# Kernel optimization log

Measured on AMD Instinct MI355X. Metric: run time of the kernel, lower is better.

The kernel has to match this reference:

```python
import jax, jax.numpy as jnp
import numpy as np

D_MODEL = 512
D_STATE = 64
D_INNER = 2 * D_MODEL   # standard Mamba expand=2
D_CONV = 4
DT_RANK = D_MODEL // 16  # 32
LN_EPS = 1e-5


def setup_inputs() -> dict:
    key = jax.random.key(0)
    ks = jax.random.split(key, 12)
    B, L = 2, 1024
    s = 0.02
    return {
        "frames": jax.random.normal(ks[0], (B, L, D_MODEL), jnp.float32),
        "gamma": jnp.ones((D_MODEL,), jnp.float32),
        "beta": jnp.zeros((D_MODEL,), jnp.float32),
        "W_in": jax.random.normal(ks[1], (D_MODEL, 2 * D_INNER), jnp.float32) * s,
        "conv_w": jax.random.normal(ks[2], (D_INNER, D_CONV), jnp.float32) * s,
        "conv_b": jnp.zeros((D_INNER,), jnp.float32),
        "W_x": jax.random.normal(ks[3], (D_INNER, DT_RANK + 2 * D_STATE), jnp.float32) * s,
        "W_dt": jax.random.normal(ks[4], (DT_RANK, D_INNER), jnp.float32) * s,
        "b_dt": jax.random.uniform(ks[5], (D_INNER,), jnp.float32, -4.0, -2.0),
        "A_log": jnp.log(jnp.broadcast_to(jnp.arange(1, D_STATE + 1, dtype=jnp.float32), (D_INNER, D_STATE))),
        "D": jnp.ones((D_INNER,), jnp.float32),
        "W_out": jax.random.normal(ks[6], (D_INNER, D_MODEL), jnp.float32) * s,
    }


def reference(frames, gamma, beta, W_in, conv_w, conv_b, W_x, W_dt, b_dt, A_log, D, W_out):
    B, L, _ = frames.shape
    d_inner = W_in.shape[1] // 2
    d_state = A_log.shape[1]
    dt_rank = W_dt.shape[0]
    d_conv = conv_w.shape[1]

    # LayerNorm
    mu = frames.mean(-1, keepdims=True)
    var = ((frames - mu) ** 2).mean(-1, keepdims=True)
    xn = (frames - mu) * jax.lax.rsqrt(var + LN_EPS) * gamma + beta

    # in_proj -> x, z
    x, z = jnp.split(xn @ W_in, 2, axis=-1)  # each (B, L, d_inner)

    # causal depthwise conv1d along time
    xc = jnp.pad(x.transpose(0, 2, 1), ((0, 0), (0, 0), (d_conv - 1, 0)))  # (B, d_inner, L+pad)
    xconv = jax.lax.conv_general_dilated(
        xc, conv_w[:, None, :], (1,), "VALID", feature_group_count=d_inner)  # (B, d_inner, L)
    x = jax.nn.silu(xconv.transpose(0, 2, 1) + conv_b)  # (B, L, d_inner)

    # input-dependent dt, B, C
    xdb = x @ W_x
    dt, Bm, Cm = jnp.split(xdb, [dt_rank, dt_rank + d_state], axis=-1)
    delta = jax.nn.softplus(dt @ W_dt + b_dt)  # (B, L, d_inner)
    A = -jnp.exp(A_log)                        # (d_inner, d_state)

    # selective scan over time
    def step(h, inp):
        d_t, B_t, C_t, x_t = inp  # (B,d_inner) (B,d_state) (B,d_state) (B,d_inner)
        dA = jnp.exp(d_t[..., None] * A)                       # (B,d_inner,d_state)
        h = h * dA + (d_t * x_t)[..., None] * B_t[:, None, :]  # (B,d_inner,d_state)
        y = jnp.einsum("bds,bs->bd", h, C_t)
        return h, y

    h0 = jnp.zeros((B, d_inner, d_state), frames.dtype)
    xs = (delta.transpose(1, 0, 2), Bm.transpose(1, 0, 2),
          Cm.transpose(1, 0, 2), x.transpose(1, 0, 2))
    _, ys = jax.lax.scan(step, h0, xs)  # (L, B, d_inner)

    y = ys.transpose(1, 0, 2) + x * D
    y = y * jax.nn.silu(z)
    return y @ W_out + frames  # residual connection
```

## Files before the change

### kernel.cpp

```cpp
#include <hip/hip_runtime.h>
#include <hip/hip_bf16.h>
#include <math.h>

constexpr int Bn     = 2;
constexpr int Lseq   = 1024;
constexpr int DM     = 512;
constexpr int DI     = 1024;
constexpr int DS     = 64;
constexpr int RNK    = 32;
constexpr int NROWS  = Bn * Lseq;
constexpr int XDBW   = RNK + 2 * DS;
constexpr int CH     = 64;
constexpr int NC     = Lseq / CH;

typedef __attribute__((ext_vector_type(4))) float floatx4;
typedef __attribute__((ext_vector_type(8))) short shortx8;

__device__ __forceinline__ float silu_f(float v) {
    return v / (1.f + __expf(-v));
}

__device__ __forceinline__ float rdl(float v, int l) {
    return __int_as_float(__builtin_amdgcn_readlane(__float_as_int(v), l));
}

__global__ void ln_kernel(const float* __restrict__ x, const float* __restrict__ g,
                          const float* __restrict__ be, __hip_bfloat16* __restrict__ xn) {
    int row = blockIdx.x;
    int tid = threadIdx.x;
    const float* xr = x + (size_t)row * DM;
    float v0 = xr[tid], v1 = xr[tid + 256];
    float s = v0 + v1, sq = v0 * v0 + v1 * v1;
    #pragma unroll
    for (int o = 1; o < 64; o <<= 1) {
        s  += __shfl_xor(s, o);
        sq += __shfl_xor(sq, o);
    }
    __shared__ float red[8];
    int w = tid >> 6;
    if ((tid & 63) == 0) { red[w] = s; red[4 + w] = sq; }
    __syncthreads();
    float ts = red[0] + red[1] + red[2] + red[3];
    float tq = red[4] + red[5] + red[6] + red[7];
    float mu  = ts * (1.f / DM);
    float var = tq * (1.f / DM) - mu * mu;
    float inv = rsqrtf(var + 1e-5f);
    __hip_bfloat16* o0 = xn + (size_t)row * DM;
    o0[tid]       = __float2bfloat16((v0 - mu) * inv * g[tid]       + be[tid]);
    o0[tid + 256] = __float2bfloat16((v1 - mu) * inv * g[tid + 256] + be[tid + 256]);
}

__global__ void transpose_cast3(const float* __restrict__ Wi, const float* __restrict__ Wo,
                                const float* __restrict__ Wx,
                                __hip_bfloat16* __restrict__ Ti, __hip_bfloat16* __restrict__ To,
                                __hip_bfloat16* __restrict__ Tx) {
    __shared__ float tile[64][65];
    int bid = blockIdx.x;
    const float* in; __hip_bfloat16* out; int R, Cc, bx, by;
    if (bid < 256)      { in = Wi; out = Ti; R = DM; Cc = 2 * DI; bx = bid & 31;        by = bid >> 5; }
    else if (bid < 384) { int b2 = bid - 256; in = Wo; out = To; R = DI; Cc = DM;   bx = b2 & 7;  by = b2 >> 3; }
    else                { int b2 = bid - 384; in = Wx; out = Tx; R = DI; Cc = XDBW; bx = b2 % 3;  by = b2 / 3; }
    int r0 = by * 64, c0 = bx * 64;
    int tid = threadIdx.x;
    #pragma unroll
    for (int i = tid; i < 4096; i += 256) {
        int r = i >> 6, c = i & 63;
        tile[r][c] = (r0 + r < R && c0 + c < Cc) ? in[(size_t)(r0 + r) * Cc + c0 + c] : 0.f;
    }
    __syncthreads();
    #pragma unroll
    for (int i = tid; i < 4096; i += 256) {
        int c = i >> 6, r = i & 63;
        if (r0 + r < R && c0 + c < Cc)
            out[(size_t)(c0 + c) * R + r0 + r] = __float2bfloat16(tile[r][c]);
    }
}

template<bool RES>
__global__ __launch_bounds__(256) void gemm_bf16(const __hip_bfloat16* __restrict__ A,
                                                 const __hip_bfloat16* __restrict__ Bt,
                                                 const float* __restrict__ Res,
                                                 float* __restrict__ C,
                                                 int M, int N, int K) {
    __shared__ __hip_bfloat16 As[128 * 32];
    __shared__ __hip_bfloat16 Bs[128 * 32];
    const int tid  = threadIdx.x;
    const int wave = tid >> 6, lane = tid & 63;
    const int m0 = blockIdx.y * 128, n0 = blockIdx.x * 128;
    const int wm = (wave >> 1) * 64, wn = (wave & 1) * 64;

    floatx4 acc[4][4] = {};

    const int arow16 = lane & 15;
    const int kgrp   = lane >> 4;

    for (int k0 = 0; k0 < K; k0 += 32) {
        #pragma unroll
        for (int r = 0; r < 2; ++r) {
            int i   = wave * 64 + r * 256 + lane;
            int row = i >> 2, seg = i & 3;
            int brow = n0 + row; if (brow >= N) brow = N - 1;
            const __hip_bfloat16* gA = A  + (size_t)(m0 + row) * K + k0 + seg * 8;
            const __hip_bfloat16* gB = Bt + (size_t)brow * K + k0 + seg * 8;
            __hip_bfloat16* lA = As + (size_t)(wave * 64 + r * 256) * 8;
            __hip_bfloat16* lB = Bs + (size_t)(wave * 64 + r * 256) * 8;
            __builtin_amdgcn_global_load_lds(
                (const __attribute__((address_space(1))) void*)gA,
                (__attribute__((address_space(3))) void*)lA, 16, 0, 0);
            __builtin_amdgcn_global_load_lds(
                (const __attribute__((address_space(1))) void*)gB,
                (__attribute__((address_space(3))) void*)lB, 16, 0, 0);
        }
        __syncthreads();

        const shortx8* Asv = (const shortx8*)As;
        const shortx8* Bsv = (const shortx8*)Bs;
        shortx8 a[4], b[4];
        #pragma unroll
        for (int i = 0; i < 4; ++i)
            a[i] = Asv[(wm + i * 16 + arow16) * 4 + kgrp];
        #pragma unroll
        for (int j = 0; j < 4; ++j)
            b[j] = Bsv[(wn + j * 16 + arow16) * 4 + kgrp];
        #pragma unroll
        for (int i = 0; i < 4; ++i)
            #pragma unroll
            for (int j = 0; j < 4; ++j)
                acc[i][j] = __builtin_amdgcn_mfma_f32_16x16x32_bf16(a[i], b[j], acc[i][j], 0, 0, 0);
        __syncthreads();
    }

    const int drow = (lane >> 4) * 4;
    const int dcol = lane & 15;
    #pragma unroll
    for (int i = 0; i < 4; ++i)
        #pragma unroll
        for (int j = 0; j < 4; ++j) {
            int rowb = m0 + wm + i * 16 + drow;
            int col  = n0 + wn + j * 16 + dcol;
            if (col < N) {
                #pragma unroll
                for (int r = 0; r < 4; ++r) {
                    size_t idx = (size_t)(rowb + r) * N + col;
                    float v = acc[i][j][r];
                    if (RES) v += Res[idx];
                    C[idx] = v;
                }
            }
        }
}

template<bool RES>
__global__ __launch_bounds__(256) void gemm_bf16_64(const __hip_bfloat16* __restrict__ A,
                                                    const __hip_bfloat16* __restrict__ Bt,
                                                    const float* __restrict__ Res,
                                                    float* __restrict__ C,
                                                    int M, int N, int K) {
    __shared__ __hip_bfloat16 As[64 * 32];
    __shared__ __hip_bfloat16 Bs[64 * 32];
    const int tid  = threadIdx.x;
    const int wave = tid >> 6, lane = tid & 63;
    const int m0 = blockIdx.y * 64, n0 = blockIdx.x * 64;
    const int wm = (wave >> 1) * 32, wn = (wave & 1) * 32;

    floatx4 acc[2][2] = {};

    const int arow16 = lane & 15;
    const int kgrp   = lane >> 4;

    for (int k0 = 0; k0 < K; k0 += 32) {
        {
            int i   = wave * 64 + lane;
            int row = i >> 2, seg = i & 3;
            int brow = n0 + row; if (brow >= N) brow = N - 1;
            const __hip_bfloat16* gA = A  + (size_t)(m0 + row) * K + k0 + seg * 8;
            const __hip_bfloat16* gB = Bt + (size_t)brow * K + k0 + seg * 8;
            __hip_bfloat16* lA = As + (size_t)(wave * 64) * 8;
            __hip_bfloat16* lB = Bs + (size_t)(wave * 64) * 8;
            __builtin_amdgcn_global_load_lds(
                (const __attribute__((address_space(1))) void*)gA,
                (__attribute__((address_space(3))) void*)lA, 16, 0, 0);
            __builtin_amdgcn_global_load_lds(
                (const __attribute__((address_space(1))) void*)gB,
                (__attribute__((address_space(3))) void*)lB, 16, 0, 0);
        }
        __syncthreads();

        const shortx8* Asv = (const shortx8*)As;
        const shortx8* Bsv = (const shortx8*)Bs;
        shortx8 a[2], b[2];
        #pragma unroll
        for (int i = 0; i < 2; ++i)
            a[i] = Asv[(wm + i * 16 + arow16) * 4 + kgrp];
        #pragma unroll
        for (int j = 0; j < 2; ++j)
            b[j] = Bsv[(wn + j * 16 + arow16) * 4 + kgrp];
        #pragma unroll
        for (int i = 0; i < 2; ++i)
            #pragma unroll
            for (int j = 0; j < 2; ++j)
                acc[i][j] = __builtin_amdgcn_mfma_f32_16x16x32_bf16(a[i], b[j], acc[i][j], 0, 0, 0);
        __syncthreads();
    }

    const int drow = (lane >> 4) * 4;
    const int dcol = lane & 15;
    #pragma unroll
    for (int i = 0; i < 2; ++i)
        #pragma unroll
        for (int j = 0; j < 2; ++j) {
            int rowb = m0 + wm + i * 16 + drow;
            int col  = n0 + wn + j * 16 + dcol;
            if (col < N) {
                #pragma unroll
                for (int r = 0; r < 4; ++r) {
                    size_t idx = (size_t)(rowb + r) * N + col;
                    float v = acc[i][j][r];
                    if (RES) v += Res[idx];
                    C[idx] = v;
                }
            }
        }
}

__global__ void conv_silu(const float* __restrict__ xz, const float* __restrict__ cw,
                          const float* __restrict__ cb, float* __restrict__ xcv,
                          __hip_bfloat16* __restrict__ xcv_bf) {
    int idx = blockIdx.x * 256 + threadIdx.x;
    int d = idx & (DI - 1);
    int bt = idx / DI;
    int t = bt & (Lseq - 1);
    int b = bt / Lseq;
    float acc = cb[d];
    #pragma unroll
    for (int k = 0; k < 4; ++k) {
        int tt = t - 3 + k;
        float xv = (tt >= 0) ? xz[((size_t)(b * Lseq + tt)) * (2 * DI) + d] : 0.f;
        acc += xv * cw[d * 4 + k];
    }
    float v = silu_f(acc);
    xcv[idx] = v;
    xcv_bf[idx] = __float2bfloat16(v);
}

__global__ void delta_kernel(const float* __restrict__ xdb, const float* __restrict__ Wdt,
                             const float* __restrict__ bdt, float* __restrict__ delta) {
    int row = blockIdx.y;
    int d = blockIdx.x * 256 + threadIdx.x;
    __shared__ float dtv[RNK];
    if (threadIdx.x < RNK) dtv[threadIdx.x] = xdb[(size_t)row * XDBW + threadIdx.x];
    __syncthreads();
    float acc = bdt[d];
    #pragma unroll
    for (int r = 0; r < RNK; ++r) acc += dtv[r] * Wdt[(size_t)r * DI + d];
    float sp = (acc > 20.f) ? acc : log1pf(__expf(acc));
    delta[(size_t)row * DI + d] = sp;
}

__global__ __launch_bounds__(512) void scan_chunk1(
        const float* __restrict__ delta, const float* __restrict__ xcv,
        const float* __restrict__ xdb, const float* __restrict__ A_log,
        float* __restrict__ hend, float* __restrict__ dsum) {
    __shared__ float Bsh[64][68];
    __shared__ float dsh[8][64];
    __shared__ float xsh[8][64];

    int blk = blockIdx.x;
    int dg  = blk & (DI / 8 - 1);
    int bc  = blk >> 7;
    int c = bc & (NC - 1), b = bc >> 4;
    int tid = threadIdx.x, w = tid >> 6, lane = tid & 63;
    int d = dg * 8 + w;
    int r0 = b * Lseq + c * CH;

    #pragma unroll
    for (int k = 0; k < 2; ++k) {
        int idx = tid + k * 512;
        int row = idx >> 4, j4 = idx & 15;
        float4 v = *(const float4*)&xdb[(size_t)(r0 + row) * XDBW + RNK + j4 * 4];
        *(float4*)&Bsh[row][j4 * 4] = v;
    }
    {
        int t = tid >> 3, ww = tid & 7;
        dsh[ww][t] = delta[(size_t)(r0 + t) * DI + dg * 8 + ww];
        xsh[ww][t] = xcv[(size_t)(r0 + t) * DI + dg * 8 + ww];
    }
    __syncthreads();

    float a = -__expf(A_log[d * DS + lane]);
    float vd  = dsh[w][lane];
    float vpx = vd * xsh[w][lane];
    float h = 0.f;
    #pragma unroll 16
    for (int t = 0; t < CH; ++t) {
        float dt_ = rdl(vd, t);
        float px  = rdl(vpx, t);
        h = h * __expf(dt_ * a) + px * Bsh[t][lane];
    }
    float S = vd;
    #pragma unroll
    for (int o = 1; o < 64; o <<= 1) S += __shfl_xor(S, o);
    size_t base = ((size_t)bc * DI + d) * 64;
    hend[base + lane] = h;
    if (lane == 0) dsum[(size_t)bc * DI + d] = S;
}

__global__ __launch_bounds__(256) void scan_stitch(
        const float* __restrict__ hend, const float* __restrict__ dsum,
        const float* __restrict__ A_log, float* __restrict__ hstart) {
    int idx = blockIdx.x * 4 + (threadIdx.x >> 6);
    int lane = threadIdx.x & 63;
    int b = idx >> 10, d = idx & (DI - 1);
    float a = -__expf(A_log[d * DS + lane]);
    float h = 0.f;
    #pragma unroll
    for (int c = 0; c < NC; ++c) {
        size_t base = ((size_t)(b * NC + c) * DI + d) * 64;
        hstart[base + lane] = h;
        float he = hend[base + lane];
        float S  = dsum[(size_t)(b * NC + c) * DI + d];
        h = he + __expf(a * S) * h;
    }
}

__global__ __launch_bounds__(512) void scan_chunk2(
        const float* __restrict__ delta, const float* __restrict__ xcv,
        const float* __restrict__ xdb, const float* __restrict__ xz,
        const float* __restrict__ A_log, const float* __restrict__ Dp,
        const float* __restrict__ hstart, __hip_bfloat16* __restrict__ y_row) {
    __shared__ unsigned int BCsh[64][65];
    __shared__ float dsh[8][64];
    __shared__ float xsh[8][64];
    __shared__ float zsh[8][64];
    __shared__ float P[8][8 * 65];

    int blk = blockIdx.x;
    int dg  = blk & (DI / 8 - 1);
    int bc  = blk >> 7;
    int c = bc & (NC - 1), b = bc >> 4;
    int tid = threadIdx.x, w = tid >> 6, lane = tid & 63;
    int d = dg * 8 + w;
    int r0 = b * Lseq + c * CH;

    #pragma unroll
    for (int k = 0; k < 2; ++k) {
        int i = tid + k * 512;
        int t = i >> 4, sg = i & 15;
        const float* rowp = &xdb[(size_t)(r0 + t) * XDBW + RNK];
        float4 bv = *(const float4*)&rowp[sg * 4];
        float4 cv = *(const float4*)&rowp[DS + sg * 4];
        uint4 pk;
        #pragma unroll
        for (int j = 0; j < 4; ++j) {
            unsigned int bb = __float_as_uint((&bv.x)[j]);
            unsigned int cc2 = __float_as_uint((&cv.x)[j]);
            (&pk.x)[j] = (cc2 & 0xFFFF0000u) | (bb >> 16);
        }
        *(uint4*)&BCsh[t][sg * 4] = pk;
    }
    {
        int t = tid >> 3, ww = tid & 7;
        dsh[ww][t] = delta[(size_t)(r0 + t) * DI + dg * 8 + ww];
        xsh[ww][t] = xcv[(size_t)(r0 + t) * DI + dg * 8 + ww];
        zsh[ww][t] = xz[(size_t)(r0 + t) * (2 * DI) + DI + dg * 8 + ww];
    }
    __syncthreads();

    float a  = -__expf(A_log[d * DS + lane]);
    float Dv = Dp[d];
    float vd  = dsh[w][lane];
    float vpx = vd * xsh[w][lane];
    float h = hstart[((size_t)bc * DI + d) * 64 + lane];
    float* Pw = P[w];
    float yreg = 0.f;
    const int tr = lane & 7, q = lane >> 3;

    #pragma unroll
    for (int t8 = 0; t8 < 8; ++t8) {
        #pragma unroll
        for (int tt = 0; tt < 8; ++tt) {
            int t = t8 * 8 + tt;
            unsigned int bcp = BCsh[t][lane];
            float Bt = __uint_as_float(bcp << 16);
            float Ct = __uint_as_float(bcp & 0xFFFF0000u);
            float dt_ = rdl(vd, t);
            float px  = rdl(vpx, t);
            h = h * __expf(dt_ * a) + px * Bt;
            Pw[tt * 65 + lane] = h * Ct;
        }
        float sacc = 0.f;
        #pragma unroll
        for (int j = 0; j < 8; ++j) sacc += Pw[tr * 65 + q * 8 + j];
        sacc += __shfl_xor(sacc, 8);
        sacc += __shfl_xor(sacc, 16);
        sacc += __shfl_xor(sacc, 32);
        if (q == t8) yreg = sacc;
    }

    float yv = (yreg + xsh[w][lane] * Dv) * silu_f(zsh[w][lane]);

    __syncthreads();
    float* T = (float*)P;
    T[lane * 9 + w] = yv;
    __syncthreads();
    {
        int t = tid >> 3, dd = tid & 7;
        float v = T[t * 9 + dd];
        y_row[(size_t)(r0 + t) * DI + dg * 8 + dd] = __float2bfloat16(v);
    }
}

extern "C" void kernel_launch(void* const* d_in, const int* in_sizes, int n_in,
                              void* d_out, int out_size, void* d_ws, size_t ws_size,
                              hipStream_t stream) {
    const float* frames = (const float*)d_in[0];
    const float* gamma  = (const float*)d_in[1];
    const float* beta   = (const float*)d_in[2];
    const float* W_in   = (const float*)d_in[3];
    const float* conv_w = (const float*)d_in[4];
    const float* conv_b = (const float*)d_in[5];
    const float* W_x    = (const float*)d_in[6];
    const float* W_dt   = (const float*)d_in[7];
    const float* b_dt   = (const float*)d_in[8];
    const float* A_log  = (const float*)d_in[9];
    const float* Dp     = (const float*)d_in[10];
    const float* W_out  = (const float*)d_in[11];
    float* out = (float*)d_out;

    char* ws = (char*)d_ws;
    __hip_bfloat16* xn_bf  = (__hip_bfloat16*)ws; ws += (size_t)NROWS * DM * 2;
    __hip_bfloat16* Wt_in  = (__hip_bfloat16*)ws; ws += (size_t)(2 * DI) * DM * 2;
    __hip_bfloat16* Wt_out = (__hip_bfloat16*)ws; ws += (size_t)DM * DI * 2;
    __hip_bfloat16* Wt_x   = (__hip_bfloat16*)ws; ws += (size_t)XDBW * DI * 2;
    __hip_bfloat16* y_row  = (__hip_bfloat16*)ws; ws += (size_t)NROWS * DI * 2;
    __hip_bfloat16* xcv_bf = (__hip_bfloat16*)ws; ws += (size_t)NROWS * DI * 2;
    float* xz     = (float*)ws;  ws += (size_t)NROWS * 2 * DI * 4;
    float* xcv    = (float*)ws;  ws += (size_t)NROWS * DI * 4;
    float* xdb    = (float*)ws;  ws += (size_t)NROWS * XDBW * 4;
    float* delta  = (float*)ws;  ws += (size_t)NROWS * DI * 4;
    float* hend   = (float*)ws;  ws += (size_t)Bn * NC * DI * 64 * 4;
    float* hstart = (float*)ws;  ws += (size_t)Bn * NC * DI * 64 * 4;
    float* dsum   = (float*)ws;  ws += (size_t)Bn * NC * DI * 4;

    transpose_cast3<<<432, 256, 0, stream>>>(W_in, W_out, W_x, Wt_in, Wt_out, Wt_x);

    ln_kernel<<<NROWS, 256, 0, stream>>>(frames, gamma, beta, xn_bf);

    gemm_bf16<false><<<dim3(2 * DI / 128, NROWS / 128), 256, 0, stream>>>(
        xn_bf, Wt_in, nullptr, xz, NROWS, 2 * DI, DM);

    conv_silu<<<(NROWS * DI) / 256, 256, 0, stream>>>(xz, conv_w, conv_b, xcv, xcv_bf);

    gemm_bf16_64<false><<<dim3((XDBW + 63) / 64, NROWS / 64), 256, 0, stream>>>(
        xcv_bf, Wt_x, nullptr, xdb, NROWS, XDBW, DI);

    delta_kernel<<<dim3(DI / 256, NROWS), 256, 0, stream>>>(xdb, W_dt, b_dt, delta);

    scan_chunk1<<<Bn * NC * (DI / 8), 512, 0, stream>>>(delta, xcv, xdb, A_log, hend, dsum);
    scan_stitch<<<Bn * DI / 4, 256, 0, stream>>>(hend, dsum, A_log, hstart);
    scan_chunk2<<<Bn * NC * (DI / 8), 512, 0, stream>>>(delta, xcv, xdb, xz, A_log, Dp, hstart, y_row);

    gemm_bf16_64<true><<<dim3(DM / 64, NROWS / 64), 256, 0, stream>>>(
        y_row, Wt_out, frames, out, NROWS, DM, DI);
}
```

Measured before the change: 246.9 us.

## Use 512-thread GEMMs with intra-block split-K for small-N projections

The in_proj GEMM now runs with 8 waves per 128x128 tile, each wave owning a 64x32 sub-tile, so every block has more waves to hide latency. The x_proj and out_proj GEMMs switch to a split-K kernel: two groups of 4 waves each handle half of K with separate LDS buffers, and the partial sums are reduced through shared memory before the store. This targets the low occupancy and long serial K loop of the small-grid GEMMs, at the cost of extra LDS use, a reduction step, and more per-block synchronisation.

```diff
diff --git a/kernel.cpp b/kernel.cpp
--- a/kernel.cpp
+++ b/kernel.cpp
@@ -77,100 +77,26 @@
 }
 
 template<bool RES>
-__global__ __launch_bounds__(256) void gemm_bf16(const __hip_bfloat16* __restrict__ A,
-                                                 const __hip_bfloat16* __restrict__ Bt,
-                                                 const float* __restrict__ Res,
-                                                 float* __restrict__ C,
-                                                 int M, int N, int K) {
+__global__ __launch_bounds__(512) void gemm_bf16_512(const __hip_bfloat16* __restrict__ A,
+                                                     const __hip_bfloat16* __restrict__ Bt,
+                                                     const float* __restrict__ Res,
+                                                     float* __restrict__ C,
+                                                     int M, int N, int K) {
     __shared__ __hip_bfloat16 As[128 * 32];
     __shared__ __hip_bfloat16 Bs[128 * 32];
     const int tid  = threadIdx.x;
     const int wave = tid >> 6, lane = tid & 63;
     const int m0 = blockIdx.y * 128, n0 = blockIdx.x * 128;
-    const int wm = (wave >> 1) * 64, wn = (wave & 1) * 64;
-
-    floatx4 acc[4][4] = {};
+    const int wm = (wave >> 2) * 64, wn = (wave & 3) * 32;
+
+    floatx4 acc[4][2] = {};
 
     const int arow16 = lane & 15;
     const int kgrp   = lane >> 4;
 
     for (int k0 = 0; k0 < K; k0 += 32) {
-        #pragma unroll
-        for (int r = 0; r < 2; ++r) {
-            int i   = wave * 64 + r * 256 + lane;
-            int row = i >> 2, seg = i & 3;
-            int brow = n0 + row; if (brow >= N) brow = N - 1;
-            const __hip_bfloat16* gA = A  + (size_t)(m0 + row) * K + k0 + seg * 8;
-            const __hip_bfloat16* gB = Bt + (size_t)brow * K + k0 + seg * 8;
-            __hip_bfloat16* lA = As + (size_t)(wave * 64 + r * 256) * 8;
-            __hip_bfloat16* lB = Bs + (size_t)(wave * 64 + r * 256) * 8;
-            __builtin_amdgcn_global_load_lds(
-                (const __attribute__((address_space(1))) void*)gA,
-                (__attribute__((address_space(3))) void*)lA, 16, 0, 0);
-            __builtin_amdgcn_global_load_lds(
-                (const __attribute__((address_space(1))) void*)gB,
-                (__attribute__((address_space(3))) void*)lB, 16, 0, 0);
-        }
-        __syncthreads();
-
-        const shortx8* Asv = (const shortx8*)As;
-        const shortx8* Bsv = (const shortx8*)Bs;
-        shortx8 a[4], b[4];
-        #pragma unroll
-        for (int i = 0; i < 4; ++i)
-            a[i] = Asv[(wm + i * 16 + arow16) * 4 + kgrp];
-        #pragma unroll
-        for (int j = 0; j < 4; ++j)
-            b[j] = Bsv[(wn + j * 16 + arow16) * 4 + kgrp];
-        #pragma unroll
-        for (int i = 0; i < 4; ++i)
-            #pragma unroll
-            for (int j = 0; j < 4; ++j)
-                acc[i][j] = __builtin_amdgcn_mfma_f32_16x16x32_bf16(a[i], b[j], acc[i][j], 0, 0, 0);
-        __syncthreads();
-    }
-
-    const int drow = (lane >> 4) * 4;
-    const int dcol = lane & 15;
-    #pragma unroll
-    for (int i = 0; i < 4; ++i)
-        #pragma unroll
-        for (int j = 0; j < 4; ++j) {
-            int rowb = m0 + wm + i * 16 + drow;
-            int col  = n0 + wn + j * 16 + dcol;
-            if (col < N) {
-                #pragma unroll
-                for (int r = 0; r < 4; ++r) {
-                    size_t idx = (size_t)(rowb + r) * N + col;
-                    float v = acc[i][j][r];
-                    if (RES) v += Res[idx];
-                    C[idx] = v;
-                }
-            }
-        }
-}
-
-template<bool RES>
-__global__ __launch_bounds__(256) void gemm_bf16_64(const __hip_bfloat16* __restrict__ A,
-                                                    const __hip_bfloat16* __restrict__ Bt,
-                                                    const float* __restrict__ Res,
-                                                    float* __restrict__ C,
-                                                    int M, int N, int K) {
-    __shared__ __hip_bfloat16 As[64 * 32];
-    __shared__ __hip_bfloat16 Bs[64 * 32];
-    const int tid  = threadIdx.x;
-    const int wave = tid >> 6, lane = tid & 63;
-    const int m0 = blockIdx.y * 64, n0 = blockIdx.x * 64;
-    const int wm = (wave >> 1) * 32, wn = (wave & 1) * 32;
-
-    floatx4 acc[2][2] = {};
-
-    const int arow16 = lane & 15;
-    const int kgrp   = lane >> 4;
-
-    for (int k0 = 0; k0 < K; k0 += 32) {
         {
-            int i   = wave * 64 + lane;
+            int i   = tid;
             int row = i >> 2, seg = i & 3;
             int brow = n0 + row; if (brow >= N) brow = N - 1;
             const __hip_bfloat16* gA = A  + (size_t)(m0 + row) * K + k0 + seg * 8;
@@ -188,15 +114,15 @@
 
         const shortx8* Asv = (const shortx8*)As;
         const shortx8* Bsv = (const shortx8*)Bs;
-        shortx8 a[2], b[2];
-        #pragma unroll
-        for (int i = 0; i < 2; ++i)
+        shortx8 a[4], b[2];
+        #pragma unroll
+        for (int i = 0; i < 4; ++i)
             a[i] = Asv[(wm + i * 16 + arow16) * 4 + kgrp];
         #pragma unroll
         for (int j = 0; j < 2; ++j)
             b[j] = Bsv[(wn + j * 16 + arow16) * 4 + kgrp];
         #pragma unroll
-        for (int i = 0; i < 2; ++i)
+        for (int i = 0; i < 4; ++i)
             #pragma unroll
             for (int j = 0; j < 2; ++j)
                 acc[i][j] = __builtin_amdgcn_mfma_f32_16x16x32_bf16(a[i], b[j], acc[i][j], 0, 0, 0);
@@ -206,7 +132,7 @@
     const int drow = (lane >> 4) * 4;
     const int dcol = lane & 15;
     #pragma unroll
-    for (int i = 0; i < 2; ++i)
+    for (int i = 0; i < 4; ++i)
         #pragma unroll
         for (int j = 0; j < 2; ++j) {
             int rowb = m0 + wm + i * 16 + drow;
@@ -221,6 +147,96 @@
                 }
             }
         }
+}
+
+template<bool RES>
+__global__ __launch_bounds__(512) void gemm64_sk(const __hip_bfloat16* __restrict__ A,
+                                                 const __hip_bfloat16* __restrict__ Bt,
+                                                 const float* __restrict__ Res,
+                                                 float* __restrict__ C,
+                                                 int M, int N, int K) {
+    __shared__ __hip_bfloat16 As[2][64 * 32];
+    __shared__ __hip_bfloat16 Bs[2][64 * 32];
+    __shared__ float red[256 * 17];
+    const int tid  = threadIdx.x;
+    const int wave = tid >> 6, lane = tid & 63;
+    const int g = wave >> 2, w2 = wave & 3;
+    const int m0 = blockIdx.y * 64, n0 = blockIdx.x * 64;
+    const int wm = (w2 >> 1) * 32, wn = (w2 & 1) * 32;
+
+    floatx4 acc[2][2] = {};
+
+    const int arow16 = lane & 15;
+    const int kgrp   = lane >> 4;
+    const int kbeg   = g * (K / 2);
+
+    for (int kk = 0; kk < K / 2; kk += 32) {
+        int k0 = kbeg + kk;
+        {
+            int i   = w2 * 64 + lane;
+            int row = i >> 2, seg = i & 3;
+            int brow = n0 + row; if (brow >= N) brow = N - 1;
+            const __hip_bfloat16* gA = A  + (size_t)(m0 + row) * K + k0 + seg * 8;
+            const __hip_bfloat16* gB = Bt + (size_t)brow * K + k0 + seg * 8;
+            __hip_bfloat16* lA = As[g] + (size_t)(w2 * 64) * 8;
+            __hip_bfloat16* lB = Bs[g] + (size_t)(w2 * 64) * 8;
+            __builtin_amdgcn_global_load_lds(
+                (const __attribute__((address_space(1))) void*)gA,
+                (__attribute__((address_space(3))) void*)lA, 16, 0, 0);
+            __builtin_amdgcn_global_load_lds(
+                (const __attribute__((address_space(1))) void*)gB,
+                (__attribute__((address_space(3))) void*)lB, 16, 0, 0);
+        }
+        __syncthreads();
+
+        const shortx8* Asv = (const shortx8*)As[g];
+        const shortx8* Bsv = (const shortx8*)Bs[g];
+        shortx8 a[2], b[2];
+        #pragma unroll
+        for (int i = 0; i < 2; ++i)
+            a[i] = Asv[(wm + i * 16 + arow16) * 4 + kgrp];
+        #pragma unroll
+        for (int j = 0; j < 2; ++j)
+            b[j] = Bsv[(wn + j * 16 + arow16) * 4 + kgrp];
+        #pragma unroll
+        for (int i = 0; i < 2; ++i)
+            #pragma unroll
+            for (int j = 0; j < 2; ++j)
+                acc[i][j] = __builtin_amdgcn_mfma_f32_16x16x32_bf16(a[i], b[j], acc[i][j], 0, 0, 0);
+        __syncthreads();
+    }
+
+    int rbase = (w2 * 64 + lane) * 17;
+    if (g == 1) {
+        #pragma unroll
+        for (int i = 0; i < 2; ++i)
+            #pragma unroll
+            for (int j = 0; j < 2; ++j)
+                *(float4*)&red[rbase + (i * 2 + j) * 4] =
+                    make_float4(acc[i][j][0], acc[i][j][1], acc[i][j][2], acc[i][j][3]);
+    }
+    __syncthreads();
+    if (g == 0) {
+        const int drow = (lane >> 4) * 4;
+        const int dcol = lane & 15;
+        #pragma unroll
+        for (int i = 0; i < 2; ++i)
+            #pragma unroll
+            for (int j = 0; j < 2; ++j) {
+                float4 part = *(const float4*)&red[rbase + (i * 2 + j) * 4];
+                int rowb = m0 + wm + i * 16 + drow;
+                int col  = n0 + wn + j * 16 + dcol;
+                if (col < N) {
+                    #pragma unroll
+                    for (int r = 0; r < 4; ++r) {
+                        size_t idx = (size_t)(rowb + r) * N + col;
+                        float v = acc[i][j][r] + (&part.x)[r];
+                        if (RES) v += Res[idx];
+                        C[idx] = v;
+                    }
+                }
+            }
+    }
 }
 
 __global__ void conv_silu(const float* __restrict__ xz, const float* __restrict__ cw,
@@ -446,12 +462,12 @@
 
     ln_kernel<<<NROWS, 256, 0, stream>>>(frames, gamma, beta, xn_bf);
 
-    gemm_bf16<false><<<dim3(2 * DI / 128, NROWS / 128), 256, 0, stream>>>(
+    gemm_bf16_512<false><<<dim3(2 * DI / 128, NROWS / 128), 512, 0, stream>>>(
         xn_bf, Wt_in, nullptr, xz, NROWS, 2 * DI, DM);
 
     conv_silu<<<(NROWS * DI) / 256, 256, 0, stream>>>(xz, conv_w, conv_b, xcv, xcv_bf);
 
-    gemm_bf16_64<false><<<dim3((XDBW + 63) / 64, NROWS / 64), 256, 0, stream>>>(
+    gemm64_sk<false><<<dim3((XDBW + 63) / 64, NROWS / 64), 512, 0, stream>>>(
         xcv_bf, Wt_x, nullptr, xdb, NROWS, XDBW, DI);
 
     delta_kernel<<<dim3(DI / 256, NROWS), 256, 0, stream>>>(xdb, W_dt, b_dt, delta);
@@ -460,6 +476,6 @@
     scan_stitch<<<Bn * DI / 4, 256, 0, stream>>>(hend, dsum, A_log, hstart);
     scan_chunk2<<<Bn * NC * (DI / 8), 512, 0, stream>>>(delta, xcv, xdb, xz, A_log, Dp, hstart, y_row);
 
-    gemm_bf16_64<true><<<dim3(DM / 64, NROWS / 64), 256, 0, stream>>>(
+    gemm64_sk<true><<<dim3(DM / 64, NROWS / 64), 512, 0, stream>>>(
         y_row, Wt_out, frames, out, NROWS, DM, DI);
 }
```

Measured after the change: 239.2 us. -3.1%, faster.
